# Optimization experiments

Measured on AMD Instinct MI355X. Metric: run time of the kernel, lower is better.

The kernel has to match this reference:

```python
import jax, jax.numpy as jnp
import numpy as np

N_NODES = 100000
N_EDGES = 600000
D = 128
BN_EPS = 1e-5


def _segment_mean(msgs, seg_ids, num_segments):
    # sum messages per destination node, divide by in-degree (0-deg nodes -> 0)
    s = jax.ops.segment_sum(msgs, seg_ids, num_segments=num_segments)
    cnt = jax.ops.segment_sum(jnp.ones((msgs.shape[0],), msgs.dtype), seg_ids,
                              num_segments=num_segments)
    return s / jnp.maximum(cnt, 1.0)[:, None]


def setup_inputs() -> dict:
    key = jax.random.key(0)
    ks = jax.random.split(key, 8)
    sc = 1.0 / np.sqrt(D)
    return {
        "node_embs": jax.random.normal(ks[0], (N_NODES, D), jnp.float32),
        "edge_embs": jax.random.normal(ks[1], (N_EDGES, D), jnp.float32),
        "W_O": jax.random.normal(ks[2], (D, D), jnp.float32) * sc,
        "b_O": jnp.zeros((D,), jnp.float32),
        "W_I": jax.random.normal(ks[3], (D, D), jnp.float32) * sc,
        "b_I": jnp.zeros((D,), jnp.float32),
        "W_S": jax.random.normal(ks[4], (D, D), jnp.float32) * sc,
        "b_S": jnp.zeros((D,), jnp.float32),
        "gamma": jnp.ones((D,), jnp.float32),
        "beta": jnp.zeros((D,), jnp.float32),
        "src": jax.random.randint(ks[5], (N_EDGES,), 0, N_NODES),
        "dst": jax.random.randint(ks[6], (N_EDGES,), 0, N_NODES),
    }


def reference(node_embs, edge_embs, W_O, b_O, W_I, b_I, W_S, b_S, gamma, beta, src, dst):
    N = node_embs.shape[0]
    # comp_opt == 'TransE': message = u_sub_e = h_src - h_edge
    # original graph: aggregate at dst -> ho
    ho = _segment_mean(node_embs[src] - edge_embs, dst, N)
    # reverse graph: edges flipped, aggregate at original src -> hi
    hi = _segment_mean(node_embs[dst] - edge_embs, src, N)
    # dropout is identity in eval; combine three projections (weights are [out,in])
    h = ((ho @ W_O.T + b_O) + (hi @ W_I.T + b_I) + (node_embs @ W_S.T + b_S)) / 3.0
    # BatchNorm1d with batch statistics (training-mode normalization, biased var)
    mu = jnp.mean(h, axis=0)
    var = jnp.mean((h - mu) ** 2, axis=0)
    h = (h - mu) * jax.lax.rsqrt(var + BN_EPS) * gamma + beta
    return h
```

## Files before the change

### kernel.cpp

```cpp
#include <hip/hip_runtime.h>
#include <hip/hip_bf16.h>

#define NN 100000
#define NE 600000
#define DD 128
#define NBLK 98

typedef __attribute__((ext_vector_type(8))) short short8_t;
typedef __attribute__((ext_vector_type(4))) float float4_t;

__device__ __forceinline__ unsigned short f2bf(float f) {
    union { float f; unsigned int i; } v; v.f = f;
    unsigned int r = v.i + 0x7fffu + ((v.i >> 16) & 1u);
    return (unsigned short)(r >> 16);
}


__global__ __launch_bounds__(256) void k_hist(
    const int* __restrict__ src, const int* __restrict__ dst,
    int* __restrict__ cnt_o, int* __restrict__ cnt_i)
{
    int e = blockIdx.x * 256 + threadIdx.x;
    if (e < NE) {
        atomicAdd(&cnt_o[dst[e]], 1);
        atomicAdd(&cnt_i[src[e]], 1);
    }
}

__global__ __launch_bounds__(256) void k_scanA(
    const int* __restrict__ cnt_o, const int* __restrict__ cnt_i,
    int* __restrict__ ptr_o, int* __restrict__ ptr_i, int* __restrict__ bsum)
{
    __shared__ int sh[256];
    const int* cnt = blockIdx.y ? cnt_i : cnt_o;
    int* ptr       = blockIdx.y ? ptr_i : ptr_o;
    int t = threadIdx.x;
    int base = blockIdx.x * 1024 + t * 4;
    int c[4];
    #pragma unroll
    for (int j = 0; j < 4; j++) c[j] = (base + j < NN) ? cnt[base + j] : 0;
    int s = c[0] + c[1] + c[2] + c[3];
    sh[t] = s;
    __syncthreads();
    for (int off = 1; off < 256; off <<= 1) {
        int v = (t >= off) ? sh[t - off] : 0;
        __syncthreads();
        sh[t] += v;
        __syncthreads();
    }
    int excl = sh[t] - s;
    int e0 = excl, e1 = e0 + c[0], e2 = e1 + c[1], e3 = e2 + c[2];
    if (base     < NN) ptr[base]     = e0;
    if (base + 1 < NN) ptr[base + 1] = e1;
    if (base + 2 < NN) ptr[base + 2] = e2;
    if (base + 3 < NN) ptr[base + 3] = e3;
    if (t == 255) bsum[blockIdx.y * 128 + blockIdx.x] = sh[255];
}

__global__ __launch_bounds__(128) void k_scanB(int* __restrict__ bsum)
{
    __shared__ int sh[128];
    int t = threadIdx.x;
    int* b = bsum + blockIdx.y * 128;
    int v = (t < NBLK) ? b[t] : 0;
    sh[t] = v;
    __syncthreads();
    for (int off = 1; off < 128; off <<= 1) {
        int u = (t >= off) ? sh[t - off] : 0;
        __syncthreads();
        sh[t] += u;
        __syncthreads();
    }
    b[t] = sh[t] - v;
}

__global__ __launch_bounds__(256) void k_scanC(
    int* __restrict__ ptr_o, int* __restrict__ ptr_i, const int* __restrict__ bsum)
{
    int* ptr = blockIdx.y ? ptr_i : ptr_o;
    int off = bsum[blockIdx.y * 128 + blockIdx.x];
    int base = blockIdx.x * 1024 + threadIdx.x * 4;
    #pragma unroll
    for (int j = 0; j < 4; j++)
        if (base + j < NN) ptr[base + j] += off;
    if (blockIdx.x == 0 && threadIdx.x == 0) ptr[NN] = NE;
}

__global__ __launch_bounds__(256) void k_fill(
    const int* __restrict__ src, const int* __restrict__ dst,
    const int* __restrict__ ptr_o, const int* __restrict__ ptr_i,
    int* __restrict__ cur_o, int* __restrict__ cur_i,
    int2* __restrict__ list_o, int2* __restrict__ list_i)
{
    int e = blockIdx.x * 256 + threadIdx.x;
    if (e < NE) {
        int s = src[e], t = dst[e];
        int p = atomicAdd(&cur_o[t], 1);
        list_o[ptr_o[t] + p] = make_int2(e, s);
        int q = atomicAdd(&cur_i[s], 1);
        list_i[ptr_i[s] + q] = make_int2(e, t);
    }
}

__global__ __launch_bounds__(256) void k_gg(
    const float* __restrict__ node, const float* __restrict__ edge,
    const int* __restrict__ ptr_o, const int* __restrict__ ptr_i,
    const int2* __restrict__ list_o, const int2* __restrict__ list_i,
    const float* __restrict__ W0, const float* __restrict__ W1, const float* __restrict__ W2,
    const float* __restrict__ b0, const float* __restrict__ b1, const float* __restrict__ b2,
    float* __restrict__ h, float* __restrict__ col_sum, float* __restrict__ col_sumsq)
{
    __shared__ unsigned short s_x[32 * 392];
    __shared__ unsigned short s_b[128 * 40];
    float* s_red = (float*)s_b;

    const int tid = threadIdx.x;
    const int n0 = blockIdx.x * 32;
    const int w  = tid >> 6;
    const int l  = tid & 63;
    const int half = l >> 5;
    const int li32 = l & 31;
    const int q  = l >> 4;
    const int li = l & 15;
    const int srow = tid >> 3;
    const int skq  = tid & 7;

    #pragma unroll
    for (int c4 = 0; c4 < 4; c4++) {
        float4 v = *(const float4*)&node[(size_t)(n0 + srow) * DD + c4 * 32 + 4 * skq];
        ushort4 o = { f2bf(v.x), f2bf(v.y), f2bf(v.z), f2bf(v.w) };
        *(ushort4*)&s_x[srow * 392 + 256 + c4 * 32 + 4 * skq] = o;
    }
    #pragma unroll
    for (int p = 0; p < 4; p++) {
        float4 v = *(const float4*)&W0[(32 * p + srow) * DD + 4 * skq];
        ushort4 o = { f2bf(v.x), f2bf(v.y), f2bf(v.z), f2bf(v.w) };
        *(ushort4*)&s_b[(32 * p + srow) * 40 + 4 * skq] = o;
    }

    for (int it = 0; it < 16; it++) {
        int tsk = w * 16 + it;
        int dirI = tsk >= 32;
        int nl = tsk & 31;
        int n = n0 + nl;
        const int* ptr   = dirI ? ptr_i  : ptr_o;
        const int2* list = dirI ? list_i : list_o;

        int p0 = ptr[n], p1 = ptr[n + 1];
        int deg = p1 - p0;
        int degc = (deg < 64) ? deg : 64;

        int2 eu = make_int2(0, 0);
        if (l < degc) eu = list[p0 + l];

        float4_t a = {0.f, 0.f, 0.f, 0.f};
        for (int t = 0; t < degc; t += 8) {
            int es[4], us[4];
            float ms[4];
            float4_t xs[4], ys[4];
            #pragma unroll
            for (int b = 0; b < 4; b++) {
                int i0 = t + 2 * b;
                int l0 = (i0     < 64) ? i0     : 0;
                int l1 = (i0 + 1 < 64) ? i0 + 1 : 0;
                int e0 = __builtin_amdgcn_readlane(eu.x, l0);
                int u0 = __builtin_amdgcn_readlane(eu.y, l0);
                int e1 = __builtin_amdgcn_readlane(eu.x, l1);
                int u1 = __builtin_amdgcn_readlane(eu.y, l1);
                es[b] = half ? e1 : e0;
                us[b] = half ? u1 : u0;
                ms[b] = (i0 + half < degc) ? 1.0f : 0.0f;
            }
            #pragma unroll
            for (int b = 0; b < 4; b++) {
                xs[b] = *((const float4_t*)(node + (size_t)us[b] * DD) + li32);
                ys[b] = *((const float4_t*)(edge + (size_t)es[b] * DD) + li32);
            }
            #pragma unroll
            for (int b = 0; b < 4; b++) {
                #pragma unroll
                for (int c = 0; c < 4; c++)
                    a[c] = fmaf(xs[b][c] - ys[b][c], ms[b], a[c]);
            }
        }
        for (int j = p0 + 64 + half; j < p1; j += 2) {
            int2 t2 = list[j];
            float4_t x = *((const float4_t*)(node + (size_t)t2.y * DD) + li32);
            float4_t y = *((const float4_t*)(edge + (size_t)t2.x * DD) + li32);
            a += x - y;
        }
        float4_t bsh;
        #pragma unroll
        for (int c = 0; c < 4; c++) bsh[c] = __shfl_xor(a[c], 32);
        a += bsh;
        float inv = (deg > 0) ? 1.0f / (float)deg : 0.0f;
        a *= inv;
        if (half == 0) {
            ushort4 o = { f2bf(a[0]), f2bf(a[1]), f2bf(a[2]), f2bf(a[3]) };
            *(ushort4*)&s_x[nl * 392 + dirI * 128 + 4 * li32] = o;
        }
    }
    __syncthreads();

    float4_t acc[2][2];
    #pragma unroll
    for (int i = 0; i < 2; i++)
        #pragma unroll
        for (int j = 0; j < 2; j++) acc[i][j] = (float4_t){0.f, 0.f, 0.f, 0.f};

    float4 wv[4];
    for (int kc = 0; kc < 12; kc++) {
        if (kc < 11) {
            int kn = kc + 1;
            const float* W = (kn < 4) ? W0 : (kn < 8) ? W1 : W2;
            int k0 = (kn & 3) * 32;
            #pragma unroll
            for (int p = 0; p < 4; p++)
                wv[p] = *(const float4*)&W[(32 * p + srow) * DD + k0 + 4 * skq];
        }
        short8_t af0 = *(const short8_t*)&s_x[li * 392 + kc * 32 + q * 8];
        short8_t af1 = *(const short8_t*)&s_x[(16 + li) * 392 + kc * 32 + q * 8];
        short8_t bf0 = *(const short8_t*)&s_b[(32 * w + li) * 40 + q * 8];
        short8_t bf1 = *(const short8_t*)&s_b[(32 * w + 16 + li) * 40 + q * 8];

        acc[0][0] = __builtin_amdgcn_mfma_f32_16x16x32_bf16(af0, bf0, acc[0][0], 0, 0, 0);
        acc[0][1] = __builtin_amdgcn_mfma_f32_16x16x32_bf16(af0, bf1, acc[0][1], 0, 0, 0);
        acc[1][0] = __builtin_amdgcn_mfma_f32_16x16x32_bf16(af1, bf0, acc[1][0], 0, 0, 0);
        acc[1][1] = __builtin_amdgcn_mfma_f32_16x16x32_bf16(af1, bf1, acc[1][1], 0, 0, 0);

        if (kc < 11) {
            __syncthreads();
            #pragma unroll
            for (int p = 0; p < 4; p++) {
                ushort4 o = { f2bf(wv[p].x), f2bf(wv[p].y), f2bf(wv[p].z), f2bf(wv[p].w) };
                *(ushort4*)&s_b[(32 * p + srow) * 40 + 4 * skq] = o;
            }
            __syncthreads();
        }
    }
    __syncthreads();

    const float third = 1.0f / 3.0f;
    #pragma unroll
    for (int j = 0; j < 2; j++) {
        int c = 32 * w + 16 * j + li;
        float bsum = b0[c] + b1[c] + b2[c];
        float s = 0.f, sq = 0.f;
        #pragma unroll
        for (int i = 0; i < 2; i++)
            #pragma unroll
            for (int reg = 0; reg < 4; reg++) {
                int r = n0 + 16 * i + q * 4 + reg;
                float v = (acc[i][j][reg] + bsum) * third;
                h[(size_t)r * DD + c] = v;
                s += v; sq += v * v;
            }
        s_red[q * 128 + c]       = s;
        s_red[512 + q * 128 + c] = sq;
    }
    __syncthreads();
    if (tid < 128) {
        float s = 0.f, sq = 0.f;
        #pragma unroll
        for (int r4 = 0; r4 < 4; r4++) {
            s  += s_red[r4 * 128 + tid];
            sq += s_red[512 + r4 * 128 + tid];
        }
        unsafeAtomicAdd(col_sum + tid, s);
        unsafeAtomicAdd(col_sumsq + tid, sq);
    }
}

__global__ void k_stats(const float* __restrict__ col_sum, const float* __restrict__ col_sumsq,
                        const float* __restrict__ gamma, const float* __restrict__ beta,
                        float* __restrict__ sc, float* __restrict__ bs)
{
    int t = threadIdx.x;
    float mu  = col_sum[t]   * (1.0f / NN);
    float var = col_sumsq[t] * (1.0f / NN) - mu * mu;
    var = fmaxf(var, 0.0f);
    float rs = rsqrtf(var + 1e-5f);
    float g = gamma[t];
    sc[t] = rs * g;
    bs[t] = beta[t] - mu * rs * g;
}

__global__ __launch_bounds__(256) void k_norm(const float* __restrict__ h,
        const float* __restrict__ sc, const float* __restrict__ bs,
        float* __restrict__ out)
{
    __shared__ float ssc[128], sbs[128];
    int tid = threadIdx.x;
    if (tid < 128) { ssc[tid] = sc[tid]; sbs[tid] = bs[tid]; }
    __syncthreads();
    size_t base = ((size_t)blockIdx.x * 256 + tid) * 4;
    float4 v = *(const float4*)(h + base);
    int j = (int)(base & 127);
    float4 o;
    o.x = fmaf(v.x, ssc[j],     sbs[j]);
    o.y = fmaf(v.y, ssc[j + 1], sbs[j + 1]);
    o.z = fmaf(v.z, ssc[j + 2], sbs[j + 2]);
    o.w = fmaf(v.w, ssc[j + 3], sbs[j + 3]);
    *(float4*)(out + base) = o;
}

extern "C" void kernel_launch(void* const* d_in, const int* in_sizes, int n_in,
                              void* d_out, int out_size, void* d_ws, size_t ws_size,
                              hipStream_t stream)
{
    const float* node  = (const float*)d_in[0];
    const float* edge  = (const float*)d_in[1];
    const float* W0    = (const float*)d_in[2];
    const float* b0    = (const float*)d_in[3];
    const float* W1    = (const float*)d_in[4];
    const float* b1    = (const float*)d_in[5];
    const float* W2    = (const float*)d_in[6];
    const float* b2    = (const float*)d_in[7];
    const float* gamma = (const float*)d_in[8];
    const float* beta  = (const float*)d_in[9];
    const int* src = (const int*)d_in[10];
    const int* dst = (const int*)d_in[11];
    float* out = (float*)d_out;

    const size_t NB = (size_t)NN * DD;
    float* h = (float*)d_ws;
    int* cnt_o = (int*)(h + NB);
    int* cnt_i = cnt_o + NN;
    int* cur_o = cnt_i + NN;
    int* cur_i = cur_o + NN;
    float* col_sum   = (float*)(cur_i + NN);
    float* col_sumsq = col_sum + DD;
    int* ptr_o = (int*)(col_sumsq + DD);
    int* ptr_i = ptr_o + (NN + 1);
    int* bsum  = ptr_i + (NN + 1);
    int2* list_o = (int2*)(bsum + 256);
    int2* list_i = list_o + NE;
    float* sc = (float*)(list_i + NE);
    float* bs = sc + DD;

    size_t zbytes = (size_t)(4 * NN + 2 * DD) * sizeof(int);
    hipMemsetAsync(cnt_o, 0, zbytes, stream);

    int egrid = (NE + 255) / 256;
    k_hist <<<egrid, 256, 0, stream>>>(src, dst, cnt_o, cnt_i);
    k_scanA<<<dim3(NBLK, 2), 256, 0, stream>>>(cnt_o, cnt_i, ptr_o, ptr_i, bsum);
    k_scanB<<<dim3(1, 2), 128, 0, stream>>>(bsum);
    k_scanC<<<dim3(NBLK, 2), 256, 0, stream>>>(ptr_o, ptr_i, bsum);
    k_fill <<<egrid, 256, 0, stream>>>(src, dst, ptr_o, ptr_i, cur_o, cur_i, list_o, list_i);
    k_gg  <<<NN / 32, 256, 0, stream>>>(node, edge, ptr_o, ptr_i, list_o, list_i,
                                        W0, W1, W2, b0, b1, b2,
                                        h, col_sum, col_sumsq);
    k_stats<<<1, 128, 0, stream>>>(col_sum, col_sumsq, gamma, beta, sc, bs);
    k_norm<<<(NN * DD) / 1024, 256, 0, stream>>>(h, sc, bs, out);
}
```

Baseline: 759.2 us.

## Pre-convert weights to MFMA-ready bf16 layout, reuse histogram ranks, fuse stats into norm

A new prep kernel converts the three weight matrices to bf16 once, laid out in MFMA fragment order. The GEMM loop in k_gg then reads B fragments straight from global memory instead of staging them through shared memory with two barriers per k-step. The A tile in shared memory now uses an XOR swizzle rather than padding. k_hist records each edge's atomic rank so k_fill no longer needs a second round of atomics, and k_stats is folded into k_norm. The trade-off is extra workspace for the rank arrays, one more small launch, and global-memory B loads in place of LDS reads.

```diff
diff --git a/kernel.cpp b/kernel.cpp
--- a/kernel.cpp
+++ b/kernel.cpp
@@ -15,15 +15,18 @@
     return (unsigned short)(r >> 16);
 }
 
+#define AX(row, cb) ((row) * 768 + ((cb) ^ (((row) & 7) << 4)))
+
 
 __global__ __launch_bounds__(256) void k_hist(
     const int* __restrict__ src, const int* __restrict__ dst,
-    int* __restrict__ cnt_o, int* __restrict__ cnt_i)
+    int* __restrict__ cnt_o, int* __restrict__ cnt_i,
+    int* __restrict__ rank_o, int* __restrict__ rank_i)
 {
     int e = blockIdx.x * 256 + threadIdx.x;
     if (e < NE) {
-        atomicAdd(&cnt_o[dst[e]], 1);
-        atomicAdd(&cnt_i[src[e]], 1);
+        rank_o[e] = atomicAdd(&cnt_o[dst[e]], 1);
+        rank_i[e] = atomicAdd(&cnt_i[src[e]], 1);
     }
 }
 
@@ -89,30 +92,46 @@
 __global__ __launch_bounds__(256) void k_fill(
     const int* __restrict__ src, const int* __restrict__ dst,
     const int* __restrict__ ptr_o, const int* __restrict__ ptr_i,
-    int* __restrict__ cur_o, int* __restrict__ cur_i,
+    const int* __restrict__ rank_o, const int* __restrict__ rank_i,
     int2* __restrict__ list_o, int2* __restrict__ list_i)
 {
     int e = blockIdx.x * 256 + threadIdx.x;
     if (e < NE) {
         int s = src[e], t = dst[e];
-        int p = atomicAdd(&cur_o[t], 1);
-        list_o[ptr_o[t] + p] = make_int2(e, s);
-        int q = atomicAdd(&cur_i[s], 1);
-        list_i[ptr_i[s] + q] = make_int2(e, t);
-    }
+        list_o[ptr_o[t] + rank_o[e]] = make_int2(e, s);
+        list_i[ptr_i[s] + rank_i[e]] = make_int2(e, t);
+    }
+}
+
+__global__ __launch_bounds__(256) void k_wprep(
+    const float* __restrict__ W0, const float* __restrict__ W1, const float* __restrict__ W2,
+    unsigned short* __restrict__ Wbf)
+{
+    int gid = blockIdx.x * 256 + threadIdx.x;
+    int m = gid >> 12;
+    int rem = gid & 4095;
+    int c = rem >> 5;
+    int k0 = (rem & 31) * 4;
+    const float* W = (m == 0) ? W0 : (m == 1) ? W1 : W2;
+    float4 v = *(const float4*)&W[c * DD + k0];
+    int kL = k0 >> 5;
+    int q = (k0 >> 3) & 3;
+    int off = k0 & 7;
+    int unit = ((m * 4 + kL) * 4 + q) * 128 + c;
+    ushort4 o = { f2bf(v.x), f2bf(v.y), f2bf(v.z), f2bf(v.w) };
+    *(ushort4*)&Wbf[unit * 8 + off] = o;
 }
 
 __global__ __launch_bounds__(256) void k_gg(
     const float* __restrict__ node, const float* __restrict__ edge,
     const int* __restrict__ ptr_o, const int* __restrict__ ptr_i,
     const int2* __restrict__ list_o, const int2* __restrict__ list_i,
-    const float* __restrict__ W0, const float* __restrict__ W1, const float* __restrict__ W2,
+    const unsigned short* __restrict__ Wbf,
     const float* __restrict__ b0, const float* __restrict__ b1, const float* __restrict__ b2,
     float* __restrict__ h, float* __restrict__ col_sum, float* __restrict__ col_sumsq)
 {
-    __shared__ unsigned short s_x[32 * 392];
-    __shared__ unsigned short s_b[128 * 40];
-    float* s_red = (float*)s_b;
+    __shared__ __align__(16) unsigned short s_x[32 * 384];
+    char* sx = (char*)s_x;
 
     const int tid = threadIdx.x;
     const int n0 = blockIdx.x * 32;
@@ -129,13 +148,7 @@
     for (int c4 = 0; c4 < 4; c4++) {
         float4 v = *(const float4*)&node[(size_t)(n0 + srow) * DD + c4 * 32 + 4 * skq];
         ushort4 o = { f2bf(v.x), f2bf(v.y), f2bf(v.z), f2bf(v.w) };
-        *(ushort4*)&s_x[srow * 392 + 256 + c4 * 32 + 4 * skq] = o;
-    }
-    #pragma unroll
-    for (int p = 0; p < 4; p++) {
-        float4 v = *(const float4*)&W0[(32 * p + srow) * DD + 4 * skq];
-        ushort4 o = { f2bf(v.x), f2bf(v.y), f2bf(v.z), f2bf(v.w) };
-        *(ushort4*)&s_b[(32 * p + srow) * 40 + 4 * skq] = o;
+        *(ushort4*)(sx + AX(srow, 512 + c4 * 64 + skq * 8)) = o;
     }
 
     for (int it = 0; it < 16; it++) {
@@ -197,7 +210,7 @@
         a *= inv;
         if (half == 0) {
             ushort4 o = { f2bf(a[0]), f2bf(a[1]), f2bf(a[2]), f2bf(a[3]) };
-            *(ushort4*)&s_x[nl * 392 + dirI * 128 + 4 * li32] = o;
+            *(ushort4*)(sx + AX(nl, dirI * 256 + li32 * 8)) = o;
         }
     }
     __syncthreads();
@@ -208,37 +221,21 @@
         #pragma unroll
         for (int j = 0; j < 2; j++) acc[i][j] = (float4_t){0.f, 0.f, 0.f, 0.f};
 
-    float4 wv[4];
+    const short8_t* Wf = (const short8_t*)Wbf;
+    #pragma unroll 4
     for (int kc = 0; kc < 12; kc++) {
-        if (kc < 11) {
-            int kn = kc + 1;
-            const float* W = (kn < 4) ? W0 : (kn < 8) ? W1 : W2;
-            int k0 = (kn & 3) * 32;
-            #pragma unroll
-            for (int p = 0; p < 4; p++)
-                wv[p] = *(const float4*)&W[(32 * p + srow) * DD + k0 + 4 * skq];
-        }
-        short8_t af0 = *(const short8_t*)&s_x[li * 392 + kc * 32 + q * 8];
-        short8_t af1 = *(const short8_t*)&s_x[(16 + li) * 392 + kc * 32 + q * 8];
-        short8_t bf0 = *(const short8_t*)&s_b[(32 * w + li) * 40 + q * 8];
-        short8_t bf1 = *(const short8_t*)&s_b[(32 * w + 16 + li) * 40 + q * 8];
+        short8_t af0 = *(const short8_t*)(sx + AX(li,      kc * 64 + q * 16));
+        short8_t af1 = *(const short8_t*)(sx + AX(16 + li, kc * 64 + q * 16));
+        short8_t bf0 = Wf[(kc * 4 + q) * 128 + 32 * w + li];
+        short8_t bf1 = Wf[(kc * 4 + q) * 128 + 32 * w + 16 + li];
 
         acc[0][0] = __builtin_amdgcn_mfma_f32_16x16x32_bf16(af0, bf0, acc[0][0], 0, 0, 0);
         acc[0][1] = __builtin_amdgcn_mfma_f32_16x16x32_bf16(af0, bf1, acc[0][1], 0, 0, 0);
         acc[1][0] = __builtin_amdgcn_mfma_f32_16x16x32_bf16(af1, bf0, acc[1][0], 0, 0, 0);
         acc[1][1] = __builtin_amdgcn_mfma_f32_16x16x32_bf16(af1, bf1, acc[1][1], 0, 0, 0);
-
-        if (kc < 11) {
-            __syncthreads();
-            #pragma unroll
-            for (int p = 0; p < 4; p++) {
-                ushort4 o = { f2bf(wv[p].x), f2bf(wv[p].y), f2bf(wv[p].z), f2bf(wv[p].w) };
-                *(ushort4*)&s_b[(32 * p + srow) * 40 + 4 * skq] = o;
-            }
-            __syncthreads();
-        }
-    }
-    __syncthreads();
+    }
+    __syncthreads();
+    float* s_red = (float*)s_x;
 
     const float third = 1.0f / 3.0f;
     #pragma unroll
@@ -271,27 +268,22 @@
     }
 }
 
-__global__ void k_stats(const float* __restrict__ col_sum, const float* __restrict__ col_sumsq,
-                        const float* __restrict__ gamma, const float* __restrict__ beta,
-                        float* __restrict__ sc, float* __restrict__ bs)
-{
-    int t = threadIdx.x;
-    float mu  = col_sum[t]   * (1.0f / NN);
-    float var = col_sumsq[t] * (1.0f / NN) - mu * mu;
-    var = fmaxf(var, 0.0f);
-    float rs = rsqrtf(var + 1e-5f);
-    float g = gamma[t];
-    sc[t] = rs * g;
-    bs[t] = beta[t] - mu * rs * g;
-}
-
 __global__ __launch_bounds__(256) void k_norm(const float* __restrict__ h,
-        const float* __restrict__ sc, const float* __restrict__ bs,
+        const float* __restrict__ col_sum, const float* __restrict__ col_sumsq,
+        const float* __restrict__ gamma, const float* __restrict__ beta,
         float* __restrict__ out)
 {
     __shared__ float ssc[128], sbs[128];
     int tid = threadIdx.x;
-    if (tid < 128) { ssc[tid] = sc[tid]; sbs[tid] = bs[tid]; }
+    if (tid < 128) {
+        float mu  = col_sum[tid]   * (1.0f / NN);
+        float var = col_sumsq[tid] * (1.0f / NN) - mu * mu;
+        var = fmaxf(var, 0.0f);
+        float rs = rsqrtf(var + 1e-5f);
+        float g = gamma[tid];
+        ssc[tid] = rs * g;
+        sbs[tid] = beta[tid] - mu * rs * g;
+    }
     __syncthreads();
     size_t base = ((size_t)blockIdx.x * 256 + tid) * 4;
     float4 v = *(const float4*)(h + base);
@@ -324,32 +316,30 @@
 
     const size_t NB = (size_t)NN * DD;
     float* h = (float*)d_ws;
-    int* cnt_o = (int*)(h + NB);
+    unsigned short* Wbf = (unsigned short*)(h + NB);
+    int* cnt_o = (int*)(Wbf + 49152);
     int* cnt_i = cnt_o + NN;
-    int* cur_o = cnt_i + NN;
-    int* cur_i = cur_o + NN;
-    float* col_sum   = (float*)(cur_i + NN);
+    float* col_sum   = (float*)(cnt_i + NN);
     float* col_sumsq = col_sum + DD;
     int* ptr_o = (int*)(col_sumsq + DD);
     int* ptr_i = ptr_o + (NN + 1);
     int* bsum  = ptr_i + (NN + 1);
-    int2* list_o = (int2*)(bsum + 256);
+    int* rank_o = bsum + 256;
+    int* rank_i = rank_o + NE;
+    int2* list_o = (int2*)(rank_i + NE);
     int2* list_i = list_o + NE;
-    float* sc = (float*)(list_i + NE);
-    float* bs = sc + DD;
-
-    size_t zbytes = (size_t)(4 * NN + 2 * DD) * sizeof(int);
+
+    size_t zbytes = (size_t)(2 * NN + 2 * DD) * sizeof(int);
     hipMemsetAsync(cnt_o, 0, zbytes, stream);
 
     int egrid = (NE + 255) / 256;
-    k_hist <<<egrid, 256, 0, stream>>>(src, dst, cnt_o, cnt_i);
+    k_wprep<<<48, 256, 0, stream>>>(W0, W1, W2, Wbf);
+    k_hist <<<egrid, 256, 0, stream>>>(src, dst, cnt_o, cnt_i, rank_o, rank_i);
     k_scanA<<<dim3(NBLK, 2), 256, 0, stream>>>(cnt_o, cnt_i, ptr_o, ptr_i, bsum);
     k_scanB<<<dim3(1, 2), 128, 0, stream>>>(bsum);
     k_scanC<<<dim3(NBLK, 2), 256, 0, stream>>>(ptr_o, ptr_i, bsum);
-    k_fill <<<egrid, 256, 0, stream>>>(src, dst, ptr_o, ptr_i, cur_o, cur_i, list_o, list_i);
+    k_fill <<<egrid, 256, 0, stream>>>(src, dst, ptr_o, ptr_i, rank_o, rank_i, list_o, list_i);
     k_gg  <<<NN / 32, 256, 0, stream>>>(node, edge, ptr_o, ptr_i, list_o, list_i,
-                                        W0, W1, W2, b0, b1, b2,
-                                        h, col_sum, col_sumsq);
-    k_stats<<<1, 128, 0, stream>>>(col_sum, col_sumsq, gamma, beta, sc, bs);
-    k_norm<<<(NN * DD) / 1024, 256, 0, stream>>>(h, sc, bs, out);
-}
+                                        Wbf, b0, b1, b2, h, col_sum, col_sumsq);
+    k_norm<<<(NN * DD) / 1024, 256, 0, stream>>>(h, col_sum, col_sumsq, gamma, beta, out);
+}
```

Result: faster. 698.3 us (-8.0%).
